# Kernel optimization log

Hardware: AMD Instinct MI355X
Metric: run time of the kernel (lower is better)

Reference implementation:

```python
import jax, jax.numpy as jnp
import numpy as np

IN_CH, OUT_CH, M1, M2 = 64, 64, 32, 32


def _powerlaw_psd_gaussian(key, exponent, n):
    """JAX port of colorednoise.powerlaw_psd_gaussian (fmin=0 default)."""
    f = jnp.fft.rfftfreq(n).astype(jnp.float32)  # [n//2+1]
    # fmin = max(0, 1/n); f[0]=0 is the only freq below it -> clamp to f[1]
    s_scale = jnp.where(f < 1.0 / n, f[1], f) ** (-exponent / 2.0)
    w = s_scale[1:]
    w = w.at[-1].multiply((1 + (n % 2)) / 2.0)  # Nyquist correction
    sigma = 2.0 * jnp.sqrt(jnp.sum(w * w)) / n
    kr, ki = jax.random.split(key)
    sr = jax.random.normal(kr, f.shape, jnp.float32) * s_scale
    si = jax.random.normal(ki, f.shape, jnp.float32) * s_scale
    if n % 2 == 0:
        si = si.at[-1].set(0.0)
        sr = sr.at[-1].multiply(jnp.sqrt(2.0))
    si = si.at[0].set(0.0)
    sr = sr.at[0].multiply(jnp.sqrt(2.0))
    return jnp.fft.irfft(sr + 1j * si, n=n) / sigma


def _compl_mul2d(t1, w, e_r, e_i, amp_r, amp_i, phi_r, phi_i, key):
    # Faithful to the torch code: stack over in-ch at dim=1 then sum dim=2
    # sums over the OUT channel axis => out[b,i,x,y] = t1[b,i,x,y]*sum_o w[i,o,x,y]
    out = t1 * jnp.sum(w, axis=1)[None]  # [B, IN_CH, M1, M2] complex
    b, c, m1, m2 = out.shape
    n = b * c * m1 * m2
    k1, k2 = jax.random.split(key)
    nr = jnp.roll(_powerlaw_psd_gaussian(k1, e_r, n), phi_r.astype(jnp.int32)) * amp_r
    ni = jnp.roll(_powerlaw_psd_gaussian(k2, e_i, n), phi_i.astype(jnp.int32)) * amp_i
    # original multiplies imag noise by amp_i twice (once in-place, once on reshape)
    noise = (nr + 1j * (ni * amp_i)).reshape(b, c, m1, m2)
    return out - noise


def _forward(x, w1, w2, exp_r, exp_i, nAmp_real, nAmp_imag, nPhase_real, nphase_imag):
    w1c = w1[..., 0] + 1j * w1[..., 1]  # [IN, OUT, M1, M2] complex64
    w2c = w2[..., 0] + 1j * w2[..., 1]
    e_r = jnp.median(exp_r)
    e_i = jnp.median(exp_i)
    amp_r = jnp.median(nAmp_real)
    amp_i = jnp.median(nAmp_imag)
    phi_r = jnp.median(nPhase_real)
    phi_i = jnp.median(nphase_imag)
    B, _, H, W = x.shape
    Wr = W // 2 + 1
    x_ft = jnp.fft.rfft2(x)  # [B, IN_CH, H, Wr]
    key = jax.random.key(42)
    kA, kB = jax.random.split(key)
    out_ft = jnp.zeros((B, OUT_CH, H, Wr), jnp.complex64)
    out_ft = out_ft.at[:, :, :M1, :M2].set(
        _compl_mul2d(x_ft[:, :, :M1, :M2], w1c, e_r, e_i, amp_r, amp_i, phi_r, phi_i, kA))
    out_ft = out_ft.at[:, :, -M1:, :M2].set(
        _compl_mul2d(x_ft[:, :, -M1:, :M2], w2c, e_r, e_i, amp_r, amp_i, phi_r, phi_i, kB))
    return jnp.fft.irfft2(out_ft, s=(H, W)).astype(jnp.float32)


def setup_inputs() -> dict:
    key = jax.random.key(0)
    ks = jax.random.split(key, 9)
    scale = 1.0 / (IN_CH * OUT_CH)
    return {
        "x": jax.random.normal(ks[0], (16, IN_CH, 256, 256), jnp.float32),
        "w1": scale * jax.random.uniform(ks[1], (IN_CH, OUT_CH, M1, M2, 2), jnp.float32),
        "w2": scale * jax.random.uniform(ks[2], (IN_CH, OUT_CH, M1, M2, 2), jnp.float32),
        "exp_r": jax.random.uniform(ks[3], (8,), jnp.float32),
        "exp_i": jax.random.uniform(ks[4], (8,), jnp.float32),
        "nAmp_real": jax.random.uniform(ks[5], (8,), jnp.float32),
        "nAmp_imag": jax.random.uniform(ks[6], (8,), jnp.float32),
        "nPhase_real": jax.random.normal(ks[7], (8,), jnp.float32),
        "nphase_imag": jax.random.normal(ks[8], (8,), jnp.float32),
    }


def reference(x, w1, w2, exp_r, exp_i, nAmp_real, nAmp_imag, nPhase_real, nphase_imag):
    return _forward(x, w1, w2, exp_r, exp_i, nAmp_real, nAmp_imag, nPhase_real, nphase_imag)
```

## Files before the change

kernel.cpp:

```cpp
#include <hip/hip_runtime.h>
#include <cstdint>

#define JPART 1
#define PART_XOR 1

constexpr uint32_t N20   = 1u << 20;
constexpr uint32_t NHALF = 1u << 19;
constexpr uint32_t NSPEC = NHALF + 1;
constexpr uint32_t SPEC_STRIDE = 524544;

struct Hdr {
  float e_r, e_i, amp_r, amp_i;
  int   phi_r, phi_i;
  float nhe_r, nhe_i;
  float scale_s[4];
};
struct KeyArgs { uint32_t k[8][2]; };

typedef __attribute__((ext_vector_type(8))) short short8;
typedef __attribute__((ext_vector_type(16))) float f32x16;

__device__ inline f32x16 zero16() {
  f32x16 v;
  #pragma unroll
  for (int i = 0; i < 16; ++i) v[i] = 0.f;
  return v;
}

__device__ inline unsigned short f2bf(float f) {
  uint32_t u = __float_as_uint(f);
  return (unsigned short)((u + 0x7fffu + ((u >> 16) & 1u)) >> 16);
}

__host__ __device__ inline void tf2x32(uint32_t k0, uint32_t k1, uint32_t x0, uint32_t x1,
                                       uint32_t& o0, uint32_t& o1) {
  const uint32_t ks0 = k0, ks1 = k1, ks2 = k0 ^ k1 ^ 0x1BD11BDAu;
  const uint32_t ks[3] = { ks0, ks1, ks2 };
  x0 += ks0; x1 += ks1;
  const int rot[2][4] = { {13,15,26,6}, {17,29,16,24} };
  for (int g = 0; g < 5; ++g) {
    const int* rr = rot[g & 1];
    for (int i = 0; i < 4; ++i) {
      x0 += x1;
      x1 = (x1 << rr[i]) | (x1 >> (32 - rr[i]));
      x1 ^= x0;
    }
    x0 += ks[(g + 1) % 3];
    x1 += ks[(g + 2) % 3] + (uint32_t)(g + 1);
  }
  o0 = x0; o1 = x1;
}

__device__ inline float erfinv_xla(float x) {
  float w = -log1pf(-x * x);
  float p;
  if (w < 5.0f) {
    w -= 2.5f;
    p = 2.81022636e-08f;
    p = fmaf(p, w, 3.43273939e-07f);
    p = fmaf(p, w, -3.5233877e-06f);
    p = fmaf(p, w, -4.39150654e-06f);
    p = fmaf(p, w, 0.00021858087f);
    p = fmaf(p, w, -0.00125372503f);
    p = fmaf(p, w, -0.00417768164f);
    p = fmaf(p, w, 0.246640727f);
    p = fmaf(p, w, 1.50140941f);
  } else {
    w = sqrtf(w) - 3.0f;
    p = -0.000200214257f;
    p = fmaf(p, w, 0.000100950558f);
    p = fmaf(p, w, 0.00134934322f);
    p = fmaf(p, w, -0.00367342844f);
    p = fmaf(p, w, 0.00573950773f);
    p = fmaf(p, w, -0.0076224613f);
    p = fmaf(p, w, 0.00943887047f);
    p = fmaf(p, w, 1.00167406f);
    p = fmaf(p, w, 2.83297682f);
  }
  return p * x;
}

__device__ inline float normal_from_bits(uint32_t bits) {
  uint32_t fb = (bits >> 9) | 0x3f800000u;
  float f = __uint_as_float(fb) - 1.0f;
  const float LO = -0.99999994f;
  float u = f * 2.0f + LO;
  u = fmaxf(LO, u);
  return 1.41421356f * erfinv_xla(u);
}

__device__ inline float sscale_f(uint32_t k, float nhe) {
  uint32_t kk = k ? k : 1u;
  return powf((float)kk * (1.0f / 1048576.0f), nhe);
}

__device__ inline float2 cmul(float2 a, float2 b) {
  return make_float2(a.x * b.x - a.y * b.y, a.x * b.y + a.y * b.x);
}
__device__ inline float2 wexp(float u) {
  float s, c; sincospif(2.0f * u, &s, &c); return make_float2(c, s);
}
__device__ inline float2 cadd(float2 a, float2 b){ return make_float2(a.x+b.x, a.y+b.y); }
__device__ inline float2 csub(float2 a, float2 b){ return make_float2(a.x-b.x, a.y-b.y); }
__device__ inline float2 cmuli(float2 a){ return make_float2(-a.y, a.x); }

__device__ inline int sA(int p) { return p ^ (((p >> 6) & 3) << 2) ^ ((p >> 8) & 3); }

__device__ inline void bfly(float2& y0, float2& y1, float2& y2, float2& y3, float2 W) {
  float2 a = cadd(y0, y2), b = csub(y0, y2);
  float2 c = cadd(y1, y3), d = cmuli(csub(y1, y3));
  float2 W2 = cmul(W, W), W3 = cmul(W2, W);
  y0 = cadd(a, c);
  y1 = cmul(cadd(b, d), W);
  y2 = cmul(csub(a, c), W2);
  y3 = cmul(csub(b, d), W3);
}

__device__ inline void fft1024_core(float2* r, float2* rc, float2* buf, int w) {
  #pragma unroll
  for (int e3 = 0; e3 < 4; ++e3) {
    float2 W = wexp((float)((e3 << 6) + w) * (1.0f / 1024.0f));
    bfly(r[e3], r[e3 + 4], r[e3 + 8], r[e3 + 12], W);
  }
  {
    float2 W = wexp((float)w * (1.0f / 256.0f));
    #pragma unroll
    for (int e4 = 0; e4 < 4; ++e4)
      bfly(r[(e4 << 2) + 0], r[(e4 << 2) + 1], r[(e4 << 2) + 2], r[(e4 << 2) + 3], W);
  }
  #pragma unroll
  for (int s = 0; s < 16; ++s) buf[sA((s << 6) + w)] = r[s];
  __syncthreads();
  {
    const int e0 = w & 3;
    const int pbase = ((w >> 4) << 8) + (((w >> 2) & 3) << 6) + e0;
    float2 rb[16];
    #pragma unroll
    for (int e2 = 0; e2 < 4; ++e2)
      #pragma unroll
      for (int e1 = 0; e1 < 4; ++e1)
        rb[(e2 << 2) + e1] = buf[sA(pbase + (e2 << 4) + (e1 << 2))];
    #pragma unroll
    for (int e1 = 0; e1 < 4; ++e1) {
      float2 W = wexp((float)((e1 << 2) + e0) * (1.0f / 64.0f));
      bfly(rb[e1], rb[e1 + 4], rb[e1 + 8], rb[e1 + 12], W);
    }
    {
      float2 W = wexp((float)e0 * (1.0f / 16.0f));
      #pragma unroll
      for (int e2 = 0; e2 < 4; ++e2)
        bfly(rb[(e2 << 2) + 0], rb[(e2 << 2) + 1], rb[(e2 << 2) + 2], rb[(e2 << 2) + 3], W);
    }
    #pragma unroll
    for (int e2 = 0; e2 < 4; ++e2)
      #pragma unroll
      for (int e1 = 0; e1 < 4; ++e1)
        buf[sA(pbase + (e2 << 4) + (e1 << 2))] = rb[(e2 << 2) + e1];
  }
  __syncthreads();
  {
    const int cbase = ((w >> 4) << 8) + (((w >> 2) & 3) << 6) + ((w & 3) << 4);
    #pragma unroll
    for (int e1 = 0; e1 < 4; ++e1)
      #pragma unroll
      for (int e0 = 0; e0 < 4; ++e0)
        rc[(e1 << 2) + e0] = buf[sA(cbase + (e1 << 2) + e0)];
    #pragma unroll
    for (int e1 = 0; e1 < 4; ++e1) {
      float2 x0 = rc[(e1 << 2)], x1 = rc[(e1 << 2) + 1], x2 = rc[(e1 << 2) + 2], x3 = rc[(e1 << 2) + 3];
      float2 a = cadd(x0, x2), b = csub(x0, x2);
      float2 c = cadd(x1, x3), d = cmuli(csub(x1, x3));
      rc[(e1 << 2)]     = cadd(a, c);
      rc[(e1 << 2) + 1] = cadd(b, d);
      rc[(e1 << 2) + 2] = csub(a, c);
      rc[(e1 << 2) + 3] = csub(b, d);
    }
  }
}

__device__ inline float med8_dev(const float* p) {
  float v[8];
  for (int i = 0; i < 8; ++i) v[i] = p[i];
  for (int i = 1; i < 8; ++i) { float key = v[i]; int j = i - 1;
    while (j >= 0 && v[j] > key) { v[j + 1] = v[j]; --j; } v[j + 1] = key; }
  return 0.5f * (v[3] + v[4]);
}

__global__ void k_scalars(Hdr* h, const float* er, const float* ei, const float* ar,
                          const float* ai, const float* pr, const float* pim) {
  if (threadIdx.x || blockIdx.x) return;
  float mer = med8_dev(er), mei = med8_dev(ei);
  h->e_r = mer; h->e_i = mei;
  h->amp_r = med8_dev(ar); h->amp_i = med8_dev(ai);
  h->phi_r = (int)med8_dev(pr);
  h->phi_i = (int)med8_dev(pim);
  h->nhe_r = -0.5f * mer; h->nhe_i = -0.5f * mei;
}

__global__ void k_sumw2(const Hdr* __restrict__ h, float* __restrict__ partials) {
  __shared__ float sr_[256], si_[256];
  const float nher = h->nhe_r, nhei = h->nhe_i;
  float sr = 0.f, si = 0.f;
  for (int j = 0; j < 4; ++j) {
    uint32_t k = (uint32_t)(blockIdx.x * 1024 + j * 256 + threadIdx.x) + 1u;
    float fk = (float)k * (1.0f / 1048576.0f);
    float wr = powf(fk, nher), wi = powf(fk, nhei);
    if (k == NHALF) { wr *= 0.5f; wi *= 0.5f; }
    sr += wr * wr; si += wi * wi;
  }
  sr_[threadIdx.x] = sr; si_[threadIdx.x] = si; __syncthreads();
  for (int off = 128; off > 0; off >>= 1) {
    if ((int)threadIdx.x < off) { sr_[threadIdx.x] += sr_[threadIdx.x + off];
                                  si_[threadIdx.x] += si_[threadIdx.x + off]; }
    __syncthreads();
  }
  if (!threadIdx.x) { partials[blockIdx.x * 2] = sr_[0]; partials[blockIdx.x * 2 + 1] = si_[0]; }
}

__global__ void k_sumw2_fin(Hdr* h, const float* partials) {
  if (threadIdx.x || blockIdx.x) return;
  float Sr = 0.f, Si = 0.f;
  for (int b = 0; b < 512; ++b) { Sr += partials[b * 2]; Si += partials[b * 2 + 1]; }
  float sig_r = 2.0f * sqrtf(Sr) * (1.0f / 1048576.0f);
  float sig_i = 2.0f * sqrtf(Si) * (1.0f / 1048576.0f);
  float s0 = h->amp_r / (sig_r * 1048576.0f);
  float s1 = (h->amp_i * h->amp_i) / (sig_i * 1048576.0f);
  h->scale_s[0] = s0; h->scale_s[1] = s1; h->scale_s[2] = s0; h->scale_s[3] = s1;
}

__global__ void k_wsum(const float* __restrict__ w1, const float* __restrict__ w2,
                       float2* __restrict__ wsum) {
  int idx = blockIdx.x * 256 + threadIdx.x;
  int sel = idx >> 16, rem = idx & 65535;
  const float* w = sel ? w2 : w1;
  int c = rem >> 10, m1 = (rem >> 5) & 31, m2 = rem & 31;
  size_t base = (size_t)c * 131072 + (size_t)m1 * 64 + (size_t)m2 * 2;
  float sr = 0.f, si = 0.f;
  for (int oc = 0; oc < 64; ++oc) { sr += w[base + (size_t)oc * 2048]; si += w[base + (size_t)oc * 2048 + 1]; }
  wsum[idx] = make_float2(sr, si);
}

__global__ void k_noise_spec(float2* __restrict__ spec, const Hdr* __restrict__ h, KeyArgs ka) {
  const int combo = blockIdx.y;
  const int s = combo >> 1, part = combo & 1;
  const float nhe = ((s & 1) == 0) ? h->nhe_r : h->nhe_i;
  const uint32_t K0 = ka.k[combo][0], K1 = ka.k[combo][1];
  float2* sp = spec + (size_t)s * SPEC_STRIDE;
  const int i = blockIdx.x * 256 + threadIdx.x;
#if JPART
  if (i >= (int)NSPEC) return;
  uint32_t o0, o1; tf2x32(K0, K1, 0u, (uint32_t)i, o0, o1);
#if PART_XOR
  uint32_t bits = o0 ^ o1;
#else
  uint32_t bits = o1;
#endif
  float val = normal_from_bits(bits) * sscale_f((uint32_t)i, nhe);
  if (i == 0 || i == (int)NHALF) val = part ? 0.0f : val * 1.41421356f;
  if (part) sp[i].y = val; else sp[i].x = val;
#else
  if (i >= 262145) return;
  uint32_t c1 = (i == 262144) ? 0u : (uint32_t)(i + 262145);
  uint32_t o0, o1; tf2x32(K0, K1, (uint32_t)i, c1, o0, o1);
  {
    uint32_t k = (uint32_t)i;
    float v = normal_from_bits(o0) * sscale_f(k, nhe);
    if (k == 0u) v = part ? 0.0f : v * 1.41421356f;
    if (part) sp[k].y = v; else sp[k].x = v;
  }
  if (i < 262144) {
    uint32_t k = (uint32_t)i + 262145u;
    float v = normal_from_bits(o1) * sscale_f(k, nhe);
    if (k == NHALF) v = part ? 0.0f : v * 1.41421356f;
    if (part) sp[k].y = v; else sp[k].x = v;
  }
#endif
}

__global__ __launch_bounds__(256) void k_fft_s1(const float2* __restrict__ spec,
                                                float2* __restrict__ G) {
  __shared__ float2 buf4[4][1024];
  const int b = blockIdx.x;
  const int lin = (b & 7) * 128 + (b >> 3);
  const int arr = lin >> 8;
  const int g = threadIdx.x >> 6, w = threadIdx.x & 63;
  const int k1 = ((lin & 255) << 2) + g;
  const float2* sp = spec + (size_t)arr * SPEC_STRIDE;

  float2 r[16], rc[16];
  #pragma unroll
  for (int s = 0; s < 16; ++s) {
    int p = (s << 6) + w;
    uint32_t k = (uint32_t)k1 + ((uint32_t)p << 10);
    float2 cv;
    if (k <= NHALF) cv = sp[k];
    else { float2 v = sp[N20 - k]; cv = make_float2(v.x, -v.y); }
    r[s] = cv;
  }
  fft1024_core(r, rc, buf4[g], w);
  float2* gp = G + ((size_t)arr << 20) + ((size_t)k1 << 10);
  const int klo = ((w & 3) << 4) + (((w >> 2) & 3) << 2) + (w >> 4);
  #pragma unroll
  for (int e1 = 0; e1 < 4; ++e1)
    #pragma unroll
    for (int e0 = 0; e0 < 4; ++e0) {
      int k = (e0 << 8) + (e1 << 6) + klo;
      float2 tw = wexp((float)(k * k1) * (1.0f / 1048576.0f));
      gp[k] = cmul(rc[(e1 << 2) + e0], tw);
    }
}

__global__ __launch_bounds__(256) void k_fft_s2(const float2* __restrict__ G,
                                                float* __restrict__ noiseP,
                                                const Hdr* __restrict__ h) {
  __shared__ float2 buf4[4][1024];
  const int b = blockIdx.x;
  const int lin = (b & 7) * 128 + (b >> 3);
  const int arr = lin >> 8;
  const int g = threadIdx.x >> 6, w = threadIdx.x & 63;
  const int j2 = ((lin & 255) << 2) + g;

  float2 r[16], rc[16];
  const float2* gp = G + ((size_t)arr << 20) + (size_t)j2;
  #pragma unroll
  for (int s = 0; s < 16; ++s) r[s] = gp[(size_t)((s << 6) + w) << 10];
  fft1024_core(r, rc, buf4[g], w);
  const float sc = h->scale_s[arr];
  float* np_ = noiseP + ((size_t)arr << 20) + ((size_t)j2 << 10);
  const int klo = ((w & 3) << 4) + (((w >> 2) & 3) << 2) + (w >> 4);
  #pragma unroll
  for (int e1 = 0; e1 < 4; ++e1)
    #pragma unroll
    for (int e0 = 0; e0 < 4; ++e0) {
      int k = (e0 << 8) + (e1 << 6) + klo;
      np_[k] = rc[(e1 << 2) + e0].x * sc;
    }
}

__global__ __launch_bounds__(256) void k_ntrans(const float* __restrict__ noiseP,
                                                float* __restrict__ noiseL,
                                                const Hdr* __restrict__ h) {
  __shared__ float tile[64][65];
  const int b = blockIdx.x;
  const int s = b >> 8, tid = b & 255;
  const int R0 = (tid >> 4) << 6;
  const int C0 = (tid & 15) << 6;
  const int t = threadIdx.x;
  const int tx = t & 63, ty = t >> 6;
  const int phi = (s & 1) ? h->phi_i : h->phi_r;
  const float* src = noiseP + ((size_t)s << 20);
  float* dst = noiseL + ((size_t)s << 20);
  #pragma unroll
  for (int i = 0; i < 16; ++i) {
    int r = (i << 2) + ty;
    tile[r][tx] = src[(size_t)((R0 + r) << 10) + (size_t)(C0 + tx)];
  }
  __syncthreads();
  #pragma unroll
  for (int i = 0; i < 16; ++i) {
    int c = (i << 2) + ty;
    int n = ((C0 + c) << 10) + R0 + tx;
    uint32_t q = (uint32_t)(n + phi) & (N20 - 1u);
    dst[q] = tile[tx][c];
  }
}

__global__ __launch_bounds__(256) void k_prep(unsigned short* __restrict__ A_E,
                                              unsigned short* __restrict__ B2T,
                                              unsigned short* __restrict__ ET,
                                              unsigned short* __restrict__ Fc,
                                              unsigned short* __restrict__ Fs,
                                              unsigned short* __restrict__ Fns) {
  int t = blockIdx.x * 256 + threadIdx.x;
  if (t < 32768) {
    int y = t >> 7, p = t & 127;
    int kyp = p & 63; int ky = (kyp < 32) ? kyp : kyp + 192;
    float s, c; sincospif(2.0f * (float)((ky * y) & 255) * (1.0f / 256.0f), &s, &c);
    A_E[t] = f2bf((p < 64) ? c : s);
  } else if (t < 49152) {
    int u = t - 32768;
    int x = u >> 6, j = u & 63, kx = j & 31;
    float s, c; sincospif(2.0f * (float)((kx * x) & 255) * (1.0f / 256.0f), &s, &c);
    float v = (j < 32) ? ((kx == 0) ? 1.0f : 2.0f * c)
                       : ((kx == 0) ? 0.0f : -2.0f * s);
    B2T[u] = f2bf(v * (1.0f / 65536.0f));
  } else if (t < 65536) {
    int u = t - 49152;
    int col = u >> 8, xx = u & 255; int kx = col & 31;
    float s, c; sincospif(2.0f * (float)((kx * xx) & 255) * (1.0f / 256.0f), &s, &c);
    ET[u] = f2bf((col < 32) ? c : -s);
  } else if (t < 114688) {
    int u = (t - 65536) & 16383;
    int which = (t - 65536) >> 14;
    int kyp = u >> 8, y = u & 255; int ky = (kyp < 32) ? kyp : kyp + 192;
    float s, c; sincospif(2.0f * (float)((ky * y) & 255) * (1.0f / 256.0f), &s, &c);
    if (which == 0) Fc[u] = f2bf(c);
    else if (which == 1) Fs[u] = f2bf(s);
    else Fns[u] = f2bf(-s);
  }
}

__global__ __launch_bounds__(256) void k_forward(const float* __restrict__ x,
    const float2* __restrict__ wsum, const float* __restrict__ noiseL,
    const unsigned short* __restrict__ ET, const unsigned short* __restrict__ Fc,
    const unsigned short* __restrict__ Fs, const unsigned short* __restrict__ Fns,
    float2* __restrict__ oftg) {
  __shared__ char lds[65536];
  char* X1T = lds + 32768;
  const int bc = blockIdx.x, t = threadIdx.x;
  const int c = bc & 63;
  const int l = t & 63, w = t >> 6, lr = l & 31, kg = l >> 5;
  const int rt = w >> 1, ct = w & 1;
  const float* xim = x + ((size_t)bc << 16);

  for (int yt = 0; yt < 4; ++yt) {
    __syncthreads();
    #pragma unroll
    for (int i = 0; i < 16; ++i) {
      int f4 = i * 256 + t;
      int r = f4 >> 6, c4 = f4 & 63;
      float4 v = *(const float4*)(xim + (size_t)(((yt << 6) + r) << 8) + (c4 << 2));
      ushort4 b4; b4.x = f2bf(v.x); b4.y = f2bf(v.y); b4.z = f2bf(v.z); b4.w = f2bf(v.w);
      int byte = ((r << 9) + (c4 << 3)) ^ ((r & 7) << 4);
      *(ushort4*)(lds + byte) = b4;
    }
    __syncthreads();
    f32x16 a1 = zero16();
    const int arow = (rt << 5) + lr;
    const int bcol = (ct << 5) + lr;
    #pragma unroll
    for (int s = 0; s < 16; ++s) {
      short8 af = *(const short8*)(lds + (((arow << 9) + (s << 5) + (kg << 4)) ^ ((arow & 7) << 4)));
      short8 bf = *(const short8*)(ET + (bcol << 8) + (s << 4) + (kg << 3));
      a1 = __builtin_amdgcn_mfma_f32_32x32x16_bf16(af, bf, a1, 0, 0, 0);
    }
    #pragma unroll
    for (int r4 = 0; r4 < 4; ++r4) {
      int y0 = (yt << 6) + (rt << 5) + (r4 << 3) + (kg << 2);
      ushort4 p4;
      p4.x = f2bf(a1[r4 * 4 + 0]); p4.y = f2bf(a1[r4 * 4 + 1]);
      p4.z = f2bf(a1[r4 * 4 + 2]); p4.w = f2bf(a1[r4 * 4 + 3]);
      int byte = ((bcol << 9) + (y0 << 1)) ^ ((bcol & 7) << 4);
      *(ushort4*)(X1T + byte) = p4;
    }
  }
  __syncthreads();

  const int re_im = w >> 1, kt = w & 1;
  const unsigned short* A1p = re_im ? Fns : Fs;
  const int b0row = (re_im ? 32 : 0) + lr;
  const int b1row = (re_im ? 0 : 32) + lr;
  const int a2row = (kt << 5) + lr;
  f32x16 a2 = zero16();
  #pragma unroll
  for (int s = 0; s < 16; ++s) {
    short8 a0f = *(const short8*)(Fc  + (a2row << 8) + (s << 4) + (kg << 3));
    short8 a1f = *(const short8*)(A1p + (a2row << 8) + (s << 4) + (kg << 3));
    short8 b0f = *(const short8*)(X1T + (((b0row << 9) + (s << 5) + (kg << 4)) ^ ((b0row & 7) << 4)));
    short8 b1f = *(const short8*)(X1T + (((b1row << 9) + (s << 5) + (kg << 4)) ^ ((b1row & 7) << 4)));
    a2 = __builtin_amdgcn_mfma_f32_32x32x16_bf16(a0f, b0f, a2, 0, 0, 0);
    a2 = __builtin_amdgcn_mfma_f32_32x32x16_bf16(a1f, b1f, a2, 0, 0, 0);
  }
  float* Osm = (float*)(lds + (re_im << 13));
  #pragma unroll
  for (int i = 0; i < 16; ++i) {
    int row = (kt << 5) + (i & 3) + ((i >> 2) << 3) + (kg << 2);
    Osm[(row << 5) + lr] = a2[i];
  }
  __syncthreads();

  const float* Ore = (const float*)lds;
  const float* Oim = (const float*)(lds + 8192);
  #pragma unroll
  for (int r = 0; r < 8; ++r) {
    int idx = (r << 8) + t;
    int kyp = idx >> 5, kx = idx & 31;
    int sel = kyp >> 5, m1 = kyp & 31;
    float2 av = make_float2(Ore[idx], Oim[idx]);
    float2 wv = wsum[((size_t)sel << 16) + (size_t)(((c << 5) | m1) << 5) + (size_t)kx];
    float2 v;
    v.x = av.x * wv.x - av.y * wv.y;
    v.y = av.x * wv.y + av.y * wv.x;
    uint32_t p = ((uint32_t)((bc << 5) | m1) << 5) | (uint32_t)kx;
    const float* nlr = noiseL + ((size_t)(sel ? 2 : 0) << 20);
    const float* nli = noiseL + ((size_t)(sel ? 3 : 1) << 20);
    v.x -= nlr[p];
    v.y -= nli[p];
    oftg[((size_t)bc << 11) + (size_t)idx] = v;
  }
}

__global__ __launch_bounds__(256) void k_inverse(const float2* __restrict__ oftg,
    const unsigned short* __restrict__ A_E, const unsigned short* __restrict__ B2T,
    float* __restrict__ out) {
  __shared__ char smem[49152];
  char* Tb = smem + 16384;
  float* ofs = (float*)(smem + 16384);

  const int bc = blockIdx.x, t = threadIdx.x;
  const int l = t & 63, w = t >> 6, lr = l & 31, kg = l >> 5;

  {
    const float4* src = (const float4*)(oftg + ((size_t)bc << 11));
    float4* dst = (float4*)ofs;
    #pragma unroll
    for (int i = 0; i < 4; ++i) dst[t + (i << 8)] = src[t + (i << 8)];
  }
  __syncthreads();

  #pragma unroll
  for (int i = 0; i < 32; ++i) {
    int idx = t + (i << 8);
    int p = idx >> 6, j = idx & 63;
    int kyp = p & 63;
    float v;
    if (p < 64) v = (j < 32) ? ofs[(kyp << 6) + (j << 1)]
                             : ofs[(kyp << 6) + ((j - 32) << 1) + 1];
    else        v = (j < 32) ? -ofs[(kyp << 6) + (j << 1) + 1]
                             : ofs[(kyp << 6) + ((j - 32) << 1)];
    int byte = ((j << 8) + (p << 1)) ^ ((j & 7) << 4);
    *(unsigned short*)(smem + byte) = f2bf(v);
  }
  __syncthreads();

  f32x16 acc[2][2];
  acc[0][0] = zero16(); acc[0][1] = zero16(); acc[1][0] = zero16(); acc[1][1] = zero16();
  #pragma unroll
  for (int s = 0; s < 8; ++s) {
    short8 af[2], bf[2];
    #pragma unroll
    for (int rt = 0; rt < 2; ++rt) {
      int row = (w << 6) + (rt << 5) + lr;
      af[rt] = *(const short8*)(A_E + (row << 7) + (s << 4) + (kg << 3));
    }
    #pragma unroll
    for (int ct = 0; ct < 2; ++ct) {
      int j = (ct << 5) + lr;
      int byte = ((j << 8) + (s << 5) + (kg << 4)) ^ ((j & 7) << 4);
      bf[ct] = *(const short8*)(smem + byte);
    }
    #pragma unroll
    for (int rt = 0; rt < 2; ++rt)
      #pragma unroll
      for (int ct = 0; ct < 2; ++ct)
        acc[rt][ct] = __builtin_amdgcn_mfma_f32_32x32x16_bf16(af[rt], bf[ct], acc[rt][ct], 0, 0, 0);
  }

  #pragma unroll
  for (int rt = 0; rt < 2; ++rt)
    #pragma unroll
    for (int ct = 0; ct < 2; ++ct)
      #pragma unroll
      for (int r = 0; r < 16; ++r) {
        int row = (w << 6) + (rt << 5) + (r & 3) + (((r >> 2) & 3) << 3) + (kg << 2);
        int col = (ct << 5) + lr;
        int byte = ((row << 7) + (col << 1)) ^ ((row & 7) << 4);
        *(unsigned short*)(Tb + byte) = f2bf(acc[rt][ct][r]);
      }
  __syncthreads();

  short8 ta[2][4];
  #pragma unroll
  for (int rt = 0; rt < 2; ++rt)
    #pragma unroll
    for (int ks = 0; ks < 4; ++ks) {
      int row = (w << 6) + (rt << 5) + lr;
      int byte = ((row << 7) + (ks << 5) + (kg << 4)) ^ ((row & 7) << 4);
      ta[rt][ks] = *(const short8*)(Tb + byte);
    }
  float* op = out + ((size_t)bc << 16);
  #pragma unroll
  for (int cc = 0; cc < 4; ++cc) {
    short8 b2[2][4];
    #pragma unroll
    for (int cx = 0; cx < 2; ++cx)
      #pragma unroll
      for (int ks = 0; ks < 4; ++ks) {
        int xx = (cc << 6) + (cx << 5) + lr;
        b2[cx][ks] = *(const short8*)(B2T + (xx << 6) + (ks << 4) + (kg << 3));
      }
    f32x16 a2[2][2];
    a2[0][0] = zero16(); a2[0][1] = zero16(); a2[1][0] = zero16(); a2[1][1] = zero16();
    #pragma unroll
    for (int ks = 0; ks < 4; ++ks)
      #pragma unroll
      for (int rt = 0; rt < 2; ++rt)
        #pragma unroll
        for (int cx = 0; cx < 2; ++cx)
          a2[rt][cx] = __builtin_amdgcn_mfma_f32_32x32x16_bf16(ta[rt][ks], b2[cx][ks], a2[rt][cx], 0, 0, 0);
    #pragma unroll
    for (int rt = 0; rt < 2; ++rt)
      #pragma unroll
      for (int cx = 0; cx < 2; ++cx)
        #pragma unroll
        for (int r = 0; r < 16; ++r) {
          int row = (w << 6) + (rt << 5) + (r & 3) + (((r >> 2) & 3) << 3) + (kg << 2);
          int xx = (cc << 6) + (cx << 5) + lr;
          op[(row << 8) + xx] = a2[rt][cx][r];
        }
  }
}

extern "C" void kernel_launch(void* const* d_in, const int* in_sizes, int n_in,
                              void* d_out, int out_size, void* d_ws, size_t ws_size,
                              hipStream_t stream) {
  (void)in_sizes; (void)n_in; (void)out_size; (void)ws_size;
  const float* x   = (const float*)d_in[0];
  const float* w1  = (const float*)d_in[1];
  const float* w2  = (const float*)d_in[2];
  const float* er  = (const float*)d_in[3];
  const float* ei  = (const float*)d_in[4];
  const float* ar  = (const float*)d_in[5];
  const float* ai  = (const float*)d_in[6];
  const float* pr  = (const float*)d_in[7];
  const float* pim = (const float*)d_in[8];
  float* out = (float*)d_out;

  char* ws = (char*)d_ws;
  Hdr*    hdr      = (Hdr*)ws;
  float*  partials = (float*)(ws + 0x1000);
  float2* wsum     = (float2*)(ws + 0x10000);
  unsigned short* A_E = (unsigned short*)(ws + 0x130000);
  unsigned short* B2T = (unsigned short*)(ws + 0x140000);
  unsigned short* ET  = (unsigned short*)(ws + 0x148000);
  unsigned short* Fc  = (unsigned short*)(ws + 0x150000);
  unsigned short* Fs  = (unsigned short*)(ws + 0x158000);
  unsigned short* Fns = (unsigned short*)(ws + 0x160000);
  float2* spec     = (float2*)(ws + 0x200000);
  float2* G        = (float2*)(ws + 0x1400000);
  float*  noiseL   = (float*)(ws + 0x1400000);
  float2* oft      = (float2*)(ws + 0x2400000);
  float*  noiseP   = (float*)(ws + 0x3400000);

  auto splitk = [](const uint32_t k[2], uint32_t a[2], uint32_t b[2]) {
#if JPART
    tf2x32(k[0], k[1], 0u, 0u, a[0], a[1]);
    tf2x32(k[0], k[1], 0u, 1u, b[0], b[1]);
#else
    uint32_t r0[2], r1[2];
    tf2x32(k[0], k[1], 0u, 2u, r0[0], r0[1]);
    tf2x32(k[0], k[1], 1u, 3u, r1[0], r1[1]);
    a[0] = r0[0]; a[1] = r1[0]; b[0] = r0[1]; b[1] = r1[1];
#endif
  };
  uint32_t root[2] = { 0u, 42u };
  uint32_t kA[2], kB[2], k1A[2], k2A[2], k1B[2], k2B[2];
  splitk(root, kA, kB);
  splitk(kA, k1A, k2A);
  splitk(kB, k1B, k2B);
  KeyArgs ka;
  splitk(k1A, ka.k[0], ka.k[1]);
  splitk(k2A, ka.k[2], ka.k[3]);
  splitk(k1B, ka.k[4], ka.k[5]);
  splitk(k2B, ka.k[6], ka.k[7]);

  hipLaunchKernelGGL(k_scalars,    dim3(1),        dim3(64),  0, stream, hdr, er, ei, ar, ai, pr, pim);
  hipLaunchKernelGGL(k_sumw2,      dim3(512),      dim3(256), 0, stream, hdr, partials);
  hipLaunchKernelGGL(k_sumw2_fin,  dim3(1),        dim3(64),  0, stream, hdr, partials);
  hipLaunchKernelGGL(k_wsum,       dim3(512),      dim3(256), 0, stream, w1, w2, wsum);
  hipLaunchKernelGGL(k_prep,       dim3(448),      dim3(256), 0, stream, A_E, B2T, ET, Fc, Fs, Fns);
  hipLaunchKernelGGL(k_noise_spec, dim3(2049, 8),  dim3(256), 0, stream, spec, hdr, ka);
  hipLaunchKernelGGL(k_fft_s1,     dim3(1024),     dim3(256), 0, stream, spec, G);
  hipLaunchKernelGGL(k_fft_s2,     dim3(1024),     dim3(256), 0, stream, G, noiseP, hdr);
  hipLaunchKernelGGL(k_ntrans,     dim3(1024),     dim3(256), 0, stream, noiseP, noiseL, hdr);
  hipLaunchKernelGGL(k_forward,    dim3(1024),     dim3(256), 0, stream, x, wsum, noiseL, ET, Fc, Fs, Fns, oft);
  hipLaunchKernelGGL(k_inverse,    dim3(1024),     dim3(256), 0, stream, oft, A_E, B2T, out);
}
```

Before: 313.3 us.

## Pack two real irfft signals into one complex FFT and transpose spectrum layout

Uses the two-for-one trick, combining two Hermitian spectra (real-noise and imag-noise) as z = X + iY so that one complex inverse FFT yields both real signals in its real and imaginary parts. This halves the number of 1M-point FFT passes and transpose blocks. The spectrum generator now writes all four components per frequency as a float4 in a k1-major transposed layout. The workspace buffers are rearranged to match. The aim is to cut the FFT and noise-generation cost, with extra index complexity for the mirrored conjugate reads.

After: 287.9 us. 8.1% less time.

```diff
diff --git a/kernel.cpp b/kernel.cpp
--- a/kernel.cpp
+++ b/kernel.cpp
@@ -6,8 +6,7 @@
 
 constexpr uint32_t N20   = 1u << 20;
 constexpr uint32_t NHALF = 1u << 19;
-constexpr uint32_t NSPEC = NHALF + 1;
-constexpr uint32_t SPEC_STRIDE = 524544;
+constexpr int SPT_STRIDE = 520;
 
 struct Hdr {
   float e_r, e_i, amp_r, amp_i;
@@ -240,65 +239,66 @@
   wsum[idx] = make_float2(sr, si);
 }
 
-__global__ void k_noise_spec(float2* __restrict__ spec, const Hdr* __restrict__ h, KeyArgs ka) {
-  const int combo = blockIdx.y;
-  const int s = combo >> 1, part = combo & 1;
-  const float nhe = ((s & 1) == 0) ? h->nhe_r : h->nhe_i;
-  const uint32_t K0 = ka.k[combo][0], K1 = ka.k[combo][1];
-  float2* sp = spec + (size_t)s * SPEC_STRIDE;
-  const int i = blockIdx.x * 256 + threadIdx.x;
-#if JPART
-  if (i >= (int)NSPEC) return;
-  uint32_t o0, o1; tf2x32(K0, K1, 0u, (uint32_t)i, o0, o1);
+__global__ void k_noise_spec(float4* __restrict__ spT, const Hdr* __restrict__ h, KeyArgs ka) {
+  const int pair = blockIdx.y;
+  const int bx = blockIdx.x;
+  const int k1 = bx >> 1, chunk = bx & 1;
+  const int k2 = (chunk << 8) + (int)threadIdx.x;
+  const float nher = h->nhe_r, nhei = h->nhe_i;
+  float4* row = spT + (size_t)pair * (1024 * SPT_STRIDE) + (size_t)k1 * SPT_STRIDE;
+  const bool extra = (k1 == 0) && (chunk == 1) && (threadIdx.x == 255);
+  const int niter = extra ? 2 : 1;
+  for (int it = 0; it < niter; ++it) {
+    const int kk2 = (it == 0) ? k2 : 512;
+    const uint32_t i = (uint32_t)k1 + ((uint32_t)kk2 << 10);
+    float vals[4];
+    #pragma unroll
+    for (int j = 0; j < 4; ++j) {
+      const uint32_t K0 = ka.k[pair * 4 + j][0], K1 = ka.k[pair * 4 + j][1];
+      uint32_t o0, o1; tf2x32(K0, K1, 0u, i, o0, o1);
 #if PART_XOR
-  uint32_t bits = o0 ^ o1;
+      uint32_t bits = o0 ^ o1;
 #else
-  uint32_t bits = o1;
+      uint32_t bits = o1;
 #endif
-  float val = normal_from_bits(bits) * sscale_f((uint32_t)i, nhe);
-  if (i == 0 || i == (int)NHALF) val = part ? 0.0f : val * 1.41421356f;
-  if (part) sp[i].y = val; else sp[i].x = val;
-#else
-  if (i >= 262145) return;
-  uint32_t c1 = (i == 262144) ? 0u : (uint32_t)(i + 262145);
-  uint32_t o0, o1; tf2x32(K0, K1, (uint32_t)i, c1, o0, o1);
-  {
-    uint32_t k = (uint32_t)i;
-    float v = normal_from_bits(o0) * sscale_f(k, nhe);
-    if (k == 0u) v = part ? 0.0f : v * 1.41421356f;
-    if (part) sp[k].y = v; else sp[k].x = v;
-  }
-  if (i < 262144) {
-    uint32_t k = (uint32_t)i + 262145u;
-    float v = normal_from_bits(o1) * sscale_f(k, nhe);
-    if (k == NHALF) v = part ? 0.0f : v * 1.41421356f;
-    if (part) sp[k].y = v; else sp[k].x = v;
-  }
-#endif
-}
-
-__global__ __launch_bounds__(256) void k_fft_s1(const float2* __restrict__ spec,
+      float nhe = (j < 2) ? nher : nhei;
+      float v = normal_from_bits(bits) * sscale_f(i, nhe);
+      if (i == 0u || i == NHALF) v = (j & 1) ? 0.0f : v * 1.41421356f;
+      vals[j] = v;
+    }
+    row[kk2] = make_float4(vals[0], vals[1], vals[2], vals[3]);
+  }
+}
+
+__global__ __launch_bounds__(256) void k_fft_s1(const float4* __restrict__ spT,
                                                 float2* __restrict__ G) {
   __shared__ float2 buf4[4][1024];
   const int b = blockIdx.x;
-  const int lin = (b & 7) * 128 + (b >> 3);
-  const int arr = lin >> 8;
+  const int lin = (b & 7) * 64 + (b >> 3);
+  const int pair = lin >> 8;
   const int g = threadIdx.x >> 6, w = threadIdx.x & 63;
   const int k1 = ((lin & 255) << 2) + g;
-  const float2* sp = spec + (size_t)arr * SPEC_STRIDE;
+  const float4* sp = spT + (size_t)pair * (1024 * SPT_STRIDE);
+  const int mrow = (1024 - k1) & 1023;
 
   float2 r[16], rc[16];
   #pragma unroll
   for (int s = 0; s < 16; ++s) {
-    int p = (s << 6) + w;
-    uint32_t k = (uint32_t)k1 + ((uint32_t)p << 10);
-    float2 cv;
-    if (k <= NHALF) cv = sp[k];
-    else { float2 v = sp[N20 - k]; cv = make_float2(v.x, -v.y); }
-    r[s] = cv;
+    int k2 = (s << 6) + w;
+    uint32_t k = (uint32_t)k1 + ((uint32_t)k2 << 10);
+    float4 f; float2 z;
+    if (k <= NHALF) {
+      f = sp[(size_t)k1 * SPT_STRIDE + k2];
+      z = make_float2(f.x - f.w, f.y + f.z);
+    } else {
+      int k2p = (k1 == 0) ? (1024 - k2) : (1023 - k2);
+      f = sp[(size_t)mrow * SPT_STRIDE + k2p];
+      z = make_float2(f.x + f.w, f.z - f.y);
+    }
+    r[s] = z;
   }
   fft1024_core(r, rc, buf4[g], w);
-  float2* gp = G + ((size_t)arr << 20) + ((size_t)k1 << 10);
+  float2* gp = G + ((size_t)pair << 20) + ((size_t)k1 << 10);
   const int klo = ((w & 3) << 4) + (((w >> 2) & 3) << 2) + (w >> 4);
   #pragma unroll
   for (int e1 = 0; e1 < 4; ++e1)
@@ -311,57 +311,60 @@
 }
 
 __global__ __launch_bounds__(256) void k_fft_s2(const float2* __restrict__ G,
-                                                float* __restrict__ noiseP,
+                                                float2* __restrict__ noiseP,
                                                 const Hdr* __restrict__ h) {
   __shared__ float2 buf4[4][1024];
   const int b = blockIdx.x;
-  const int lin = (b & 7) * 128 + (b >> 3);
-  const int arr = lin >> 8;
+  const int lin = (b & 7) * 64 + (b >> 3);
+  const int pair = lin >> 8;
   const int g = threadIdx.x >> 6, w = threadIdx.x & 63;
   const int j2 = ((lin & 255) << 2) + g;
 
   float2 r[16], rc[16];
-  const float2* gp = G + ((size_t)arr << 20) + (size_t)j2;
+  const float2* gp = G + ((size_t)pair << 20) + (size_t)j2;
   #pragma unroll
   for (int s = 0; s < 16; ++s) r[s] = gp[(size_t)((s << 6) + w) << 10];
   fft1024_core(r, rc, buf4[g], w);
-  const float sc = h->scale_s[arr];
-  float* np_ = noiseP + ((size_t)arr << 20) + ((size_t)j2 << 10);
+  const float scr = h->scale_s[0], sci = h->scale_s[1];
+  float2* np_ = noiseP + ((size_t)pair << 20) + ((size_t)j2 << 10);
   const int klo = ((w & 3) << 4) + (((w >> 2) & 3) << 2) + (w >> 4);
   #pragma unroll
   for (int e1 = 0; e1 < 4; ++e1)
     #pragma unroll
     for (int e0 = 0; e0 < 4; ++e0) {
       int k = (e0 << 8) + (e1 << 6) + klo;
-      np_[k] = rc[(e1 << 2) + e0].x * sc;
-    }
-}
-
-__global__ __launch_bounds__(256) void k_ntrans(const float* __restrict__ noiseP,
+      np_[k] = make_float2(rc[(e1 << 2) + e0].x * scr, rc[(e1 << 2) + e0].y * sci);
+    }
+}
+
+__global__ __launch_bounds__(256) void k_ntrans(const float2* __restrict__ noiseP,
                                                 float* __restrict__ noiseL,
                                                 const Hdr* __restrict__ h) {
-  __shared__ float tile[64][65];
+  __shared__ float tr[64][65];
+  __shared__ float ti[64][65];
   const int b = blockIdx.x;
-  const int s = b >> 8, tid = b & 255;
+  const int pair = b >> 8, tid = b & 255;
   const int R0 = (tid >> 4) << 6;
   const int C0 = (tid & 15) << 6;
   const int t = threadIdx.x;
   const int tx = t & 63, ty = t >> 6;
-  const int phi = (s & 1) ? h->phi_i : h->phi_r;
-  const float* src = noiseP + ((size_t)s << 20);
-  float* dst = noiseL + ((size_t)s << 20);
+  const int phir = h->phi_r, phii = h->phi_i;
+  const float2* src = noiseP + ((size_t)pair << 20);
+  float* dstr = noiseL + ((size_t)(pair * 2) << 20);
+  float* dsti = noiseL + ((size_t)(pair * 2 + 1) << 20);
   #pragma unroll
   for (int i = 0; i < 16; ++i) {
     int r = (i << 2) + ty;
-    tile[r][tx] = src[(size_t)((R0 + r) << 10) + (size_t)(C0 + tx)];
+    float2 v = src[(size_t)((R0 + r) << 10) + (size_t)(C0 + tx)];
+    tr[r][tx] = v.x; ti[r][tx] = v.y;
   }
   __syncthreads();
   #pragma unroll
   for (int i = 0; i < 16; ++i) {
     int c = (i << 2) + ty;
     int n = ((C0 + c) << 10) + R0 + tx;
-    uint32_t q = (uint32_t)(n + phi) & (N20 - 1u);
-    dst[q] = tile[tx][c];
+    dstr[(uint32_t)(n + phir) & (N20 - 1u)] = tr[tx][c];
+    dsti[(uint32_t)(n + phii) & (N20 - 1u)] = ti[tx][c];
   }
 }
 
@@ -626,11 +629,12 @@
   unsigned short* Fc  = (unsigned short*)(ws + 0x150000);
   unsigned short* Fs  = (unsigned short*)(ws + 0x158000);
   unsigned short* Fns = (unsigned short*)(ws + 0x160000);
-  float2* spec     = (float2*)(ws + 0x200000);
+  float4* spT      = (float4*)(ws + 0x200000);
   float2* G        = (float2*)(ws + 0x1400000);
-  float*  noiseL   = (float*)(ws + 0x1400000);
-  float2* oft      = (float2*)(ws + 0x2400000);
-  float*  noiseP   = (float*)(ws + 0x3400000);
+  float2* oft      = (float2*)(ws + 0x1400000);
+  float2* noiseP   = (float2*)(ws + 0x2400000);
+  float*  noiseL   = (float*)(ws + 0x3400000);
+
 
   auto splitk = [](const uint32_t k[2], uint32_t a[2], uint32_t b[2]) {
 #if JPART
@@ -659,10 +663,10 @@
   hipLaunchKernelGGL(k_sumw2_fin,  dim3(1),        dim3(64),  0, stream, hdr, partials);
   hipLaunchKernelGGL(k_wsum,       dim3(512),      dim3(256), 0, stream, w1, w2, wsum);
   hipLaunchKernelGGL(k_prep,       dim3(448),      dim3(256), 0, stream, A_E, B2T, ET, Fc, Fs, Fns);
-  hipLaunchKernelGGL(k_noise_spec, dim3(2049, 8),  dim3(256), 0, stream, spec, hdr, ka);
-  hipLaunchKernelGGL(k_fft_s1,     dim3(1024),     dim3(256), 0, stream, spec, G);
-  hipLaunchKernelGGL(k_fft_s2,     dim3(1024),     dim3(256), 0, stream, G, noiseP, hdr);
-  hipLaunchKernelGGL(k_ntrans,     dim3(1024),     dim3(256), 0, stream, noiseP, noiseL, hdr);
+  hipLaunchKernelGGL(k_noise_spec, dim3(2048, 2),  dim3(256), 0, stream, spT, hdr, ka);
+  hipLaunchKernelGGL(k_fft_s1,     dim3(512),      dim3(256), 0, stream, spT, G);
+  hipLaunchKernelGGL(k_fft_s2,     dim3(512),      dim3(256), 0, stream, G, noiseP, hdr);
+  hipLaunchKernelGGL(k_ntrans,     dim3(512),      dim3(256), 0, stream, noiseP, noiseL, hdr);
   hipLaunchKernelGGL(k_forward,    dim3(1024),     dim3(256), 0, stream, x, wsum, noiseL, ET, Fc, Fs, Fns, oft);
   hipLaunchKernelGGL(k_inverse,    dim3(1024),     dim3(256), 0, stream, oft, A_E, B2T, out);
 }
```
